# Kernel tuning notes

Measured on AMD Instinct MI355X. Metric: run time of the kernel, lower is better.

## Reference

```python
import jax, jax.numpy as jnp
import numpy as np

B, S, E, H = 2, 2048, 1024, 16
D = E // H  # head_dim = 64


def setup_inputs() -> dict:
    key = jax.random.key(0)
    ks = jax.random.split(key, 9)
    sc = 1.0 / np.sqrt(E)
    return {
        "x": jax.random.normal(ks[0], (B, S, E), dtype=jnp.float32),
        "Wq": jax.random.normal(ks[1], (E, E), dtype=jnp.float32) * sc,
        "bq": jnp.zeros((E,), dtype=jnp.float32),
        "Wk": jax.random.normal(ks[2], (E, E), dtype=jnp.float32) * sc,
        "bk": jnp.zeros((E,), dtype=jnp.float32),
        "Wv": jax.random.normal(ks[3], (E, E), dtype=jnp.float32) * sc,
        "bv": jnp.zeros((E,), dtype=jnp.float32),
        "Wo": jax.random.normal(ks[4], (E, E), dtype=jnp.float32) * sc,
        "bo": jnp.zeros((E,), dtype=jnp.float32),
    }


def reference(x, Wq, bq, Wk, bk, Wv, bv, Wo, bo):
    b, s, e = x.shape
    # projections: [B,S,E] -> [B,H,S,D]
    def heads(w, bias):
        return (x @ w + bias).reshape(b, s, H, D).transpose(0, 2, 1, 3)
    q, k, v = heads(Wq, bq), heads(Wk, bk), heads(Wv, bv)
    # scores [B,H,S,S]
    scores = jnp.einsum("bhqd,bhkd->bhqk", q, k) / jnp.sqrt(jnp.float32(D))
    causal = jnp.tril(jnp.ones((s, s), dtype=bool))
    scores = jnp.where(causal[None, None], scores, -jnp.inf)
    weights = jax.nn.softmax(scores, axis=-1)
    out = jnp.einsum("bhqk,bhkd->bhqd", weights, v)
    out = out.transpose(0, 2, 1, 3).reshape(b, s, e)
    return out @ Wo + bo
```

## Files before the change

kernel.cpp:

```cpp
#include <hip/hip_runtime.h>
#include <hip/hip_bf16.h>

#define B_SZ 2
#define S_LEN 2048
#define E_DIM 1024
#define NH 16
#define DH 64
#define M_ROWS (B_SZ * S_LEN)
#define QB 128
#define KVB 64

typedef __attribute__((ext_vector_type(8))) short short8;
typedef __attribute__((ext_vector_type(4))) float floatx4;

static __device__ __forceinline__ unsigned short f2bf(float f) {
    __hip_bfloat16 h = __float2bfloat16(f);
    return *reinterpret_cast<unsigned short*>(&h);
}
static __device__ __forceinline__ float bf2f(unsigned short u) {
    unsigned int v = ((unsigned int)u) << 16;
    return __builtin_bit_cast(float, v);
}

static __device__ __forceinline__ void gl2lds16(const void* g, void* l) {
    __builtin_amdgcn_global_load_lds((const __attribute__((address_space(1))) void*)g,
                                     (__attribute__((address_space(3))) void*)l, 16, 0, 0);
}

__global__ __launch_bounds__(256) void cvt_f32_bf16(const float* __restrict__ x,
                                                    unsigned short* __restrict__ y, int n) {
    int i = (blockIdx.x * 256 + threadIdx.x) * 4;
    if (i >= n) return;
    float4 v = *reinterpret_cast<const float4*>(x + i);
    ushort4 o;
    o.x = f2bf(v.x); o.y = f2bf(v.y); o.z = f2bf(v.z); o.w = f2bf(v.w);
    *reinterpret_cast<ushort4*>(y + i) = o;
}

__global__ __launch_bounds__(256) void transpose_w4(const float* __restrict__ W0,
                                                    const float* __restrict__ W1,
                                                    const float* __restrict__ W2,
                                                    const float* __restrict__ W3,
                                                    unsigned short* __restrict__ T0,
                                                    unsigned short* __restrict__ T1,
                                                    unsigned short* __restrict__ T2,
                                                    unsigned short* __restrict__ T3) {
    __shared__ float tile[32][33];
    int z = blockIdx.z;
    const float* W = (z == 0) ? W0 : (z == 1) ? W1 : (z == 2) ? W2 : W3;
    unsigned short* Wt = (z == 0) ? T0 : (z == 1) ? T1 : (z == 2) ? T2 : T3;
    int tx = threadIdx.x, ty = threadIdx.y;
    int bx = blockIdx.x * 32, by = blockIdx.y * 32;
#pragma unroll
    for (int i = 0; i < 32; i += 8)
        tile[ty + i][tx] = W[(size_t)(by + ty + i) * E_DIM + bx + tx];
    __syncthreads();
#pragma unroll
    for (int i = 0; i < 32; i += 8)
        Wt[(size_t)(bx + ty + i) * E_DIM + by + tx] = f2bf(tile[tx][ty + i]);
}

template <int NI>
static __device__ __forceinline__ void gemm_tile_mainloop(
    const unsigned short* __restrict__ A, const unsigned short* __restrict__ Bt,
    int mBase, int nBase, char* ldsA, char* ldsB, floatx4 (&acc)[4][NI]) {
    const int K = E_DIM;
    int t = threadIdx.x;
    int w = t >> 6, lane = t & 63;
    int lr = lane & 15, lh = lane >> 4;
    int wm = w >> 1, wn = w & 1;
    const char* Ab = (const char*)A;
    const char* Bb = (const char*)Bt;
    int srow = t >> 3;
    int scb = ((t & 7) << 4) ^ ((srow & 7) << 4);

#pragma unroll
    for (int mi = 0; mi < 4; mi++)
#pragma unroll
        for (int ni = 0; ni < NI; ni++) acc[mi][ni] = (floatx4){0.f, 0.f, 0.f, 0.f};

    for (int kt = 0; kt < K / 64; ++kt) {
        int k0 = kt * 64;
#pragma unroll
        for (int i = 0; i < 4; i++)
            gl2lds16(Ab + (size_t)(mBase + i * 32 + srow) * (K * 2) + k0 * 2 + scb,
                     ldsA + i * 4096 + t * 16);
#pragma unroll
        for (int i = 0; i < NI; i++)
            gl2lds16(Bb + (size_t)(nBase + i * 32 + srow) * (K * 2) + k0 * 2 + scb,
                     ldsB + i * 4096 + t * 16);
        __syncthreads();
#pragma unroll
        for (int ks = 0; ks < 2; ks++) {
            short8 af[4], bf[NI];
#pragma unroll
            for (int mi = 0; mi < 4; mi++) {
                int row = wm * 64 + mi * 16 + lr;
                af[mi] = *reinterpret_cast<const short8*>(
                    ldsA + ((row * 128 + ks * 64 + lh * 16) ^ ((row & 7) << 4)));
            }
#pragma unroll
            for (int ni = 0; ni < NI; ni++) {
                int row = wn * (NI * 16) + ni * 16 + lr;
                bf[ni] = *reinterpret_cast<const short8*>(
                    ldsB + ((row * 128 + ks * 64 + lh * 16) ^ ((row & 7) << 4)));
            }
#pragma unroll
            for (int mi = 0; mi < 4; mi++)
#pragma unroll
                for (int ni = 0; ni < NI; ni++)
                    acc[mi][ni] = __builtin_amdgcn_mfma_f32_16x16x32_bf16(af[mi], bf[ni],
                                                                          acc[mi][ni], 0, 0, 0);
        }
        __syncthreads();
    }
}

#define QSCALE 0.18033688011112042f

__global__ __launch_bounds__(256) void gemm_qkv(const unsigned short* __restrict__ Xb,
                                                const unsigned short* __restrict__ Wqt,
                                                const unsigned short* __restrict__ Wkt,
                                                const unsigned short* __restrict__ Wvt,
                                                const float* __restrict__ bq,
                                                const float* __restrict__ bk,
                                                const float* __restrict__ bv,
                                                unsigned short* __restrict__ Qg,
                                                unsigned short* __restrict__ Kg,
                                                unsigned short* __restrict__ Vtg) {
    __shared__ __align__(16) char smem[34816];
    char* ldsA = smem;
    char* ldsB = smem + 16384;

    int bid = blockIdx.y * 24 + blockIdx.x;
    int xcd = bid & 7, ii = bid >> 3;
    int lx = ii % 12, ly = ii / 12;
    int xx = (xcd & 1) * 12 + lx;
    int yy = ((xcd >> 1) << 3) + ly;
    int wsel = xx >> 3;
    int nBase = (xx & 7) << 7;
    int mBase = yy << 7;
    const unsigned short* Bt = (wsel == 0) ? Wqt : (wsel == 1) ? Wkt : Wvt;
    const float* bias = (wsel == 0) ? bq : (wsel == 1) ? bk : bv;

    floatx4 acc[4][4];
    gemm_tile_mainloop<4>(Xb, Bt, mBase, nBase, ldsA, ldsB, acc);

    int w = threadIdx.x >> 6, lane = threadIdx.x & 63;
    int lr = lane & 15, lh = lane >> 4;
    int wm = w >> 1, wn = w & 1;
    int b_ = mBase >> 11, s0 = mBase & (S_LEN - 1);

    if (wsel == 2) {
#pragma unroll
        for (int mi = 0; mi < 4; mi++) {
            int s_ = s0 + wm * 64 + mi * 16 + lh * 4;
#pragma unroll
            for (int ni = 0; ni < 4; ni++) {
                int nl = nBase + wn * 64 + ni * 16 + lr;
                int h = nl >> 6, d = nl & 63;
                float bb = bias[nl];
                ushort4 pk;
                pk.x = f2bf(acc[mi][ni][0] + bb);
                pk.y = f2bf(acc[mi][ni][1] + bb);
                pk.z = f2bf(acc[mi][ni][2] + bb);
                pk.w = f2bf(acc[mi][ni][3] + bb);
                *reinterpret_cast<ushort4*>(
                    &Vtg[((size_t)(b_ * NH + h) * DH + d) * S_LEN + s_]) = pk;
            }
        }
    } else {
        unsigned short* et = reinterpret_cast<unsigned short*>(smem);
        unsigned short* O = wsel ? Kg : Qg;
        float scale = wsel ? 1.0f : QSCALE;
#pragma unroll
        for (int mi = 0; mi < 4; mi++)
#pragma unroll
            for (int ni = 0; ni < 4; ni++) {
                int nl = wn * 64 + ni * 16 + lr;
                float bb = bias[nBase + nl];
#pragma unroll
                for (int r = 0; r < 4; r++) {
                    int ml = wm * 64 + mi * 16 + lh * 4 + r;
                    int q = ((ml >> 2) & 3) << 3;
                    et[ml * 136 + (nl ^ q)] = f2bf((acc[mi][ni][r] + bb) * scale);
                }
            }
        __syncthreads();
#pragma unroll
        for (int c = 0; c < 8; c++) {
            int id = c * 256 + threadIdx.x;
            int ml = id >> 4, nc = id & 15;
            int q = ((ml >> 2) & 3) << 3;
            short8 vv = *reinterpret_cast<const short8*>(&et[ml * 136 + ((nc * 8) ^ q)]);
            int n = nBase + nc * 8;
            int h = n >> 6, d = n & 63;
            *reinterpret_cast<short8*>(
                &O[((size_t)(b_ * NH + h) * S_LEN + (s0 + ml)) * DH + d]) = vv;
        }
    }
}

__global__ __launch_bounds__(256) void gemm_o(const unsigned short* __restrict__ Og,
                                              const unsigned short* __restrict__ Wot,
                                              const float* __restrict__ bo,
                                              float* __restrict__ out) {
    __shared__ __align__(16) char ldsA[16384];
    __shared__ __align__(16) char ldsB[8192];
    int bid = blockIdx.y * 16 + blockIdx.x;
    int xcd = bid & 7, ii = bid >> 3;
    int xx = ii & 15;
    int yy = (xcd << 2) | (ii >> 4);
    int nBase = xx << 6;
    int mBase = yy << 7;

    floatx4 acc[4][2];
    gemm_tile_mainloop<2>(Og, Wot, mBase, nBase, ldsA, ldsB, acc);

    int w = threadIdx.x >> 6, lane = threadIdx.x & 63;
    int lr = lane & 15, lh = lane >> 4;
    int wm = w >> 1, wn = w & 1;
#pragma unroll
    for (int mi = 0; mi < 4; mi++)
#pragma unroll
        for (int ni = 0; ni < 2; ni++)
#pragma unroll
            for (int r = 0; r < 4; r++) {
                int m = mBase + wm * 64 + mi * 16 + lh * 4 + r;
                int n = nBase + wn * 32 + ni * 16 + lr;
                out[(size_t)m * E_DIM + n] = acc[mi][ni][r] + bo[n];
            }
}

__global__ __launch_bounds__(256) void attn_fwd(const unsigned short* __restrict__ Qg,
                                                const unsigned short* __restrict__ Kg,
                                                const unsigned short* __restrict__ Vtg,
                                                unsigned short* __restrict__ Og,
                                                unsigned short* __restrict__ Opart,
                                                float* __restrict__ lpart) {
    __shared__ __align__(16) char kt_lds[2][KVB * 128];
    __shared__ __align__(16) char vt_lds[2][KVB * 128];
    __shared__ __align__(16) unsigned short p_lds[4][32][72];

    int bid = blockIdx.y * 24 + blockIdx.x;
    int xcd = bid & 7, ii = bid >> 3;
    int idx = ii % 24;
    int bh = (xcd << 2) + ii / 24;

    int qb, kt_lo, kt_hi, chunk;
    bool split;
    if (idx < 16) {
        split = true;
        qb = 8 + (idx & 7);
        chunk = idx >> 3;
        if (chunk == 0) { kt_lo = 0; kt_hi = qb; }
        else            { kt_lo = qb + 1; kt_hi = 2 * qb + 1; }
    } else {
        split = false; chunk = 0;
        qb = 23 - idx;
        kt_lo = 0; kt_hi = 2 * qb + 1;
    }

    int w = threadIdx.x >> 6, lane = threadIdx.x & 63;
    int lr = lane & 15, lh = lane >> 4;
    int q0 = qb * QB + w * 32;

    const char* Kb = (const char*)(Kg + (size_t)bh * S_LEN * DH);
    const char* Vb = (const char*)(Vtg + (size_t)bh * DH * S_LEN);
    const unsigned short* Qb = Qg + (size_t)bh * S_LEN * DH;

    int wi0 = w * 2;
    int srow0 = wi0 * 8 + (lane >> 3);
    int scol = (lane & 7) << 4;

    auto stage = [&](int buf, int kt) {
        int kv0 = kt * KVB;
#pragma unroll
        for (int i = 0; i < 2; ++i) {
            int row = srow0 + i * 8;
            int colb = scol ^ ((row & 7) << 4);
            gl2lds16(Kb + (size_t)(kv0 + row) * 128 + colb,
                     kt_lds[buf] + (wi0 + i) * 1024);
            gl2lds16(Vb + (size_t)row * (S_LEN * 2) + (size_t)kv0 * 2 + colb,
                     vt_lds[buf] + (wi0 + i) * 1024);
        }
    };

    short8 aq[2][2];
#pragma unroll
    for (int m = 0; m < 2; m++)
#pragma unroll
        for (int ks = 0; ks < 2; ks++)
            aq[m][ks] = *reinterpret_cast<const short8*>(
                Qb + (size_t)(q0 + m * 16 + lr) * DH + ks * 32 + lh * 8);

    floatx4 oacc[2][4];
    float lsum[2][4];
#pragma unroll
    for (int m = 0; m < 2; m++) {
#pragma unroll
        for (int dt = 0; dt < 4; dt++) oacc[m][dt] = (floatx4){0.f, 0.f, 0.f, 0.f};
#pragma unroll
        for (int r = 0; r < 4; r++) lsum[m][r] = 0.f;
    }

    stage(0, kt_lo);
    __syncthreads();
    int buf = 0;

    for (int kt = kt_lo; kt <= kt_hi; ++kt) {
        if (kt < kt_hi) stage(buf ^ 1, kt + 1);
        int kv0 = kt * KVB;
        bool skip = (kv0 > q0 + 31);
        if (!skip) {
            const char* Kt = kt_lds[buf];
            const char* Vt = vt_lds[buf];
            floatx4 sacc[2][4];
#pragma unroll
            for (int m = 0; m < 2; m++)
#pragma unroll
                for (int nt = 0; nt < 4; nt++) sacc[m][nt] = (floatx4){0.f, 0.f, 0.f, 0.f};
#pragma unroll
            for (int ks = 0; ks < 2; ks++)
#pragma unroll
                for (int nt = 0; nt < 4; nt++) {
                    int row = nt * 16 + lr;
                    int addr = (row * 128 + ks * 64 + lh * 16) ^ ((row & 7) << 4);
                    short8 bk = *reinterpret_cast<const short8*>(Kt + addr);
#pragma unroll
                    for (int m = 0; m < 2; m++)
                        sacc[m][nt] = __builtin_amdgcn_mfma_f32_16x16x32_bf16(
                            aq[m][ks], bk, sacc[m][nt], 0, 0, 0);
                }
            if (kv0 + KVB - 1 > q0) {
#pragma unroll
                for (int m = 0; m < 2; m++)
#pragma unroll
                    for (int nt = 0; nt < 4; nt++)
#pragma unroll
                        for (int r = 0; r < 4; r++) {
                            int qrow = q0 + m * 16 + lh * 4 + r;
                            int kcol = kv0 + nt * 16 + lr;
                            if (kcol > qrow) sacc[m][nt][r] = -1e30f;
                        }
            }
#pragma unroll
            for (int m = 0; m < 2; m++) {
                float rs[4] = {0.f, 0.f, 0.f, 0.f};
#pragma unroll
                for (int nt = 0; nt < 4; nt++)
#pragma unroll
                    for (int r = 0; r < 4; r++) {
                        float p = __builtin_amdgcn_exp2f(sacc[m][nt][r]);
                        rs[r] += p;
                        p_lds[w][m * 16 + lh * 4 + r][nt * 16 + lr] = f2bf(p);
                    }
#pragma unroll
                for (int r = 0; r < 4; r++) lsum[m][r] += rs[r];
            }
            asm volatile("s_waitcnt lgkmcnt(0)" ::: "memory");
            short8 pa[2][2];
#pragma unroll
            for (int m = 0; m < 2; m++)
#pragma unroll
                for (int ks = 0; ks < 2; ks++)
                    pa[m][ks] = *reinterpret_cast<const short8*>(
                        &p_lds[w][m * 16 + lr][ks * 32 + lh * 8]);
#pragma unroll
            for (int ks = 0; ks < 2; ks++)
#pragma unroll
                for (int dt = 0; dt < 4; dt++) {
                    int row = dt * 16 + lr;
                    int addr = (row * 128 + ks * 64 + lh * 16) ^ ((row & 7) << 4);
                    short8 bv = *reinterpret_cast<const short8*>(Vt + addr);
#pragma unroll
                    for (int m = 0; m < 2; m++)
                        oacc[m][dt] = __builtin_amdgcn_mfma_f32_16x16x32_bf16(
                            pa[m][ks], bv, oacc[m][dt], 0, 0, 0);
                }
        }
        __syncthreads();
        buf ^= 1;
    }

#pragma unroll
    for (int m = 0; m < 2; m++)
#pragma unroll
        for (int msk = 1; msk < 16; msk <<= 1)
#pragma unroll
            for (int r = 0; r < 4; r++) lsum[m][r] += __shfl_xor(lsum[m][r], msk);

    if (split) {
        int pi = ((bh << 3) + (qb - 8)) * 2 + chunk;
        unsigned short* Op = Opart + (size_t)pi * (QB * DH);
        float* lp = lpart + (size_t)pi * QB;
#pragma unroll
        for (int m = 0; m < 2; m++) {
#pragma unroll
            for (int r = 0; r < 4; r++) {
                int row = w * 32 + m * 16 + lh * 4 + r;
#pragma unroll
                for (int dt = 0; dt < 4; dt++)
                    Op[row * DH + dt * 16 + lr] = f2bf(oacc[m][dt][r]);
                if (lr == r) lp[row] = lsum[m][r];
            }
        }
    } else {
        int b_ = bh >> 4, h_ = bh & 15;
#pragma unroll
        for (int m = 0; m < 2; m++)
#pragma unroll
            for (int r = 0; r < 4; r++) {
                float inv = 1.f / lsum[m][r];
                int srow = q0 + m * 16 + lh * 4 + r;
#pragma unroll
                for (int dt = 0; dt < 4; dt++)
                    Og[((size_t)b_ * S_LEN + srow) * E_DIM + h_ * 64 + dt * 16 + lr] =
                        f2bf(oacc[m][dt][r] * inv);
            }
    }
}

__global__ __launch_bounds__(256) void attn_reduce(const unsigned short* __restrict__ Opart,
                                                   const float* __restrict__ lpart,
                                                   unsigned short* __restrict__ Og) {
    int bh = blockIdx.x;
    int qt = blockIdx.y;
    int t = threadIdx.x;
    int cg = t & 7, r0 = t >> 3;
    int pi0 = ((bh << 3) + qt) * 2;
    const unsigned short* A = Opart + (size_t)pi0 * (QB * DH);
    const unsigned short* Bp = A + (QB * DH);
    const float* lA = lpart + (size_t)pi0 * QB;
    const float* lB = lA + QB;
    int b_ = bh >> 4, h_ = bh & 15;
    int qrow0 = (8 + qt) * QB;
#pragma unroll
    for (int rr = 0; rr < 4; rr++) {
        int row = r0 + rr * 32;
        float inv = 1.f / (lA[row] + lB[row]);
        short8 va = *reinterpret_cast<const short8*>(A + row * DH + cg * 8);
        short8 vb = *reinterpret_cast<const short8*>(Bp + row * DH + cg * 8);
        short8 o;
#pragma unroll
        for (int j = 0; j < 8; j++)
            o[j] = (short)f2bf((bf2f((unsigned short)va[j]) + bf2f((unsigned short)vb[j])) * inv);
        *reinterpret_cast<short8*>(Og + ((size_t)b_ * S_LEN + qrow0 + row) * E_DIM +
                                   h_ * 64 + cg * 8) = o;
    }
}

extern "C" void kernel_launch(void* const* d_in, const int* in_sizes, int n_in,
                              void* d_out, int out_size, void* d_ws, size_t ws_size,
                              hipStream_t stream) {
    const float* x  = (const float*)d_in[0];
    const float* Wq = (const float*)d_in[1];
    const float* bq = (const float*)d_in[2];
    const float* Wk = (const float*)d_in[3];
    const float* bk = (const float*)d_in[4];
    const float* Wv = (const float*)d_in[5];
    const float* bv = (const float*)d_in[6];
    const float* Wo = (const float*)d_in[7];
    const float* bo = (const float*)d_in[8];
    float* out = (float*)d_out;

    const size_t NX = (size_t)M_ROWS * E_DIM;
    const size_t NW = (size_t)E_DIM * E_DIM;
    unsigned short* ws  = (unsigned short*)d_ws;
    unsigned short* Xb  = ws;
    unsigned short* Wqt = Xb + NX;
    unsigned short* Wkt = Wqt + NW;
    unsigned short* Wvt = Wkt + NW;
    unsigned short* Wot = Wvt + NW;
    unsigned short* Qg  = Wot + NW;
    unsigned short* Kg  = Qg + NX;
    unsigned short* Vtg = Kg + NX;
    unsigned short* Og  = Vtg + NX;
    unsigned short* Opart = Og + NX;
    float* lpart = (float*)(Opart + (size_t)512 * QB * DH);

    cvt_f32_bf16<<<dim3((unsigned)(NX / (256 * 4))), dim3(256), 0, stream>>>(x, Xb, (int)NX);
    transpose_w4<<<dim3(32, 32, 4), dim3(32, 8), 0, stream>>>(Wq, Wk, Wv, Wo,
                                                              Wqt, Wkt, Wvt, Wot);

    gemm_qkv<<<dim3(24, M_ROWS / 128), 256, 0, stream>>>(Xb, Wqt, Wkt, Wvt, bq, bk, bv,
                                                         Qg, Kg, Vtg);

    attn_fwd<<<dim3(24, B_SZ * NH), 256, 0, stream>>>(Qg, Kg, Vtg, Og, Opart, lpart);
    attn_reduce<<<dim3(B_SZ * NH, 8), 256, 0, stream>>>(Opart, lpart, Og);

    gemm_o<<<dim3(E_DIM / 64, M_ROWS / 128), 256, 0, stream>>>(Og, Wot, bo, out);
}
```

Baseline: 116.1 us.

## Fuse prep kernels and rewrite QKV GEMM with 256x256 double-buffered tiles

Merges the x conversion and the weight transpose into one prep launch. Replaces the QKV projection with a 512-thread kernel that computes Wcat·X^T in 256x256 tiles, using double-buffered LDS with the next tile's global loads interleaved between MFMA phases. It relies on Wqt/Wkt/Wvt being contiguous in the workspace so they act as one concatenated weight matrix. The larger tiles raise data reuse and cut the launch count, at the cost of 128KB of LDS, more registers, only 192 blocks, and new epilogue paths for the Q/K and transposed V layouts.

```diff
diff --git a/kernel.cpp b/kernel.cpp
--- a/kernel.cpp
+++ b/kernel.cpp
@@ -27,30 +27,36 @@
                                      (__attribute__((address_space(3))) void*)l, 16, 0, 0);
 }
 
-__global__ __launch_bounds__(256) void cvt_f32_bf16(const float* __restrict__ x,
-                                                    unsigned short* __restrict__ y, int n) {
-    int i = (blockIdx.x * 256 + threadIdx.x) * 4;
-    if (i >= n) return;
-    float4 v = *reinterpret_cast<const float4*>(x + i);
-    ushort4 o;
-    o.x = f2bf(v.x); o.y = f2bf(v.y); o.z = f2bf(v.z); o.w = f2bf(v.w);
-    *reinterpret_cast<ushort4*>(y + i) = o;
-}
-
-__global__ __launch_bounds__(256) void transpose_w4(const float* __restrict__ W0,
-                                                    const float* __restrict__ W1,
-                                                    const float* __restrict__ W2,
-                                                    const float* __restrict__ W3,
-                                                    unsigned short* __restrict__ T0,
-                                                    unsigned short* __restrict__ T1,
-                                                    unsigned short* __restrict__ T2,
-                                                    unsigned short* __restrict__ T3) {
+#define WAIT_VM0() asm volatile("s_waitcnt vmcnt(0)" ::: "memory")
+#define WAIT_LGKM0() asm volatile("s_waitcnt lgkmcnt(0)" ::: "memory")
+
+__global__ __launch_bounds__(256) void prep(const float* __restrict__ x,
+                                            unsigned short* __restrict__ Xb,
+                                            const float* __restrict__ W0,
+                                            const float* __restrict__ W1,
+                                            const float* __restrict__ W2,
+                                            const float* __restrict__ W3,
+                                            unsigned short* __restrict__ T0,
+                                            unsigned short* __restrict__ T1,
+                                            unsigned short* __restrict__ T2,
+                                            unsigned short* __restrict__ T3) {
     __shared__ float tile[32][33];
-    int z = blockIdx.z;
+    int bid = blockIdx.x;
+    int t = threadIdx.x;
+    if (bid < 4096) {
+        int i = (bid * 256 + t) * 4;
+        float4 v = *reinterpret_cast<const float4*>(x + i);
+        ushort4 o;
+        o.x = f2bf(v.x); o.y = f2bf(v.y); o.z = f2bf(v.z); o.w = f2bf(v.w);
+        *reinterpret_cast<ushort4*>(Xb + i) = o;
+        return;
+    }
+    int u = bid - 4096;
+    int z = u >> 10, rest = u & 1023;
+    int bx = (rest & 31) * 32, by = (rest >> 5) * 32;
     const float* W = (z == 0) ? W0 : (z == 1) ? W1 : (z == 2) ? W2 : W3;
     unsigned short* Wt = (z == 0) ? T0 : (z == 1) ? T1 : (z == 2) ? T2 : T3;
-    int tx = threadIdx.x, ty = threadIdx.y;
-    int bx = blockIdx.x * 32, by = blockIdx.y * 32;
+    int tx = t & 31, ty = t >> 5;
 #pragma unroll
     for (int i = 0; i < 32; i += 8)
         tile[ty + i][tx] = W[(size_t)(by + ty + i) * E_DIM + bx + tx];
@@ -58,6 +64,189 @@
 #pragma unroll
     for (int i = 0; i < 32; i += 8)
         Wt[(size_t)(bx + ty + i) * E_DIM + by + tx] = f2bf(tile[tx][ty + i]);
+}
+
+#define QSCALE 0.18033688011112042f
+
+__global__ __launch_bounds__(512, 2) void gemm_qkv8(const unsigned short* __restrict__ Wcat,
+                                                    const unsigned short* __restrict__ Xb,
+                                                    const float* __restrict__ bq,
+                                                    const float* __restrict__ bk,
+                                                    const float* __restrict__ bv,
+                                                    unsigned short* __restrict__ Qg,
+                                                    unsigned short* __restrict__ Kg,
+                                                    unsigned short* __restrict__ Vtg) {
+    __shared__ __align__(16) char lds[2][2][32768];
+
+    int t = threadIdx.x;
+    int b = blockIdx.x;
+    int xcd = b & 7, ii = b >> 3;
+    int it = (xcd & 3) * 3 + (ii >> 3);
+    int jt = (xcd >> 2) * 8 + (ii & 7);
+    int iBase = it << 8, jBase = jt << 8;
+
+    int w = t >> 6, lane = t & 63;
+    int lr = lane & 15, lh = lane >> 4;
+    int wm = w >> 2, wn = w & 3;
+
+    int srow = t >> 3;
+    int scbx = ((t & 7) << 4) ^ ((srow & 7) << 4);
+
+    const char* Ab = (const char*)Wcat;
+    const char* Bb = (const char*)Xb;
+
+    floatx4 acc[8][4];
+#pragma unroll
+    for (int i = 0; i < 8; i++)
+#pragma unroll
+        for (int j = 0; j < 4; j++) acc[i][j] = (floatx4){0.f, 0.f, 0.f, 0.f};
+
+    auto stageA = [&](int buf, int kt) {
+        int k0b = kt << 7;
+#pragma unroll
+        for (int c = 0; c < 4; c++)
+            gl2lds16(Ab + (size_t)(iBase + c * 64 + srow) * 2048 + k0b + scbx,
+                     &lds[buf][0][c * 8192 + t * 16]);
+    };
+    auto stageB = [&](int buf, int kt) {
+        int k0b = kt << 7;
+#pragma unroll
+        for (int c = 0; c < 4; c++)
+            gl2lds16(Bb + (size_t)(jBase + c * 64 + srow) * 2048 + k0b + scbx,
+                     &lds[buf][1][c * 8192 + t * 16]);
+    };
+
+    short8 af[4][2], bf[4][2];
+    auto rdA = [&](int buf, int qm) {
+#pragma unroll
+        for (int mi = 0; mi < 4; mi++)
+#pragma unroll
+            for (int ks = 0; ks < 2; ks++) {
+                int row = wm * 128 + qm * 64 + mi * 16 + lr;
+                af[mi][ks] = *reinterpret_cast<const short8*>(
+                    &lds[buf][0][(row * 128 + ks * 64 + lh * 16) ^ ((row & 7) << 4)]);
+            }
+    };
+    auto rdB = [&](int buf, int qn) {
+#pragma unroll
+        for (int ni = 0; ni < 2; ni++)
+#pragma unroll
+            for (int ks = 0; ks < 2; ks++) {
+                int row = wn * 64 + qn * 32 + ni * 16 + lr;
+                bf[qn * 2 + ni][ks] = *reinterpret_cast<const short8*>(
+                    &lds[buf][1][(row * 128 + ks * 64 + lh * 16) ^ ((row & 7) << 4)]);
+            }
+    };
+    auto mfma16 = [&](int qm, int qn) {
+        __builtin_amdgcn_s_setprio(1);
+#pragma unroll
+        for (int mi = 0; mi < 4; mi++)
+#pragma unroll
+            for (int ni = 0; ni < 2; ni++)
+#pragma unroll
+                for (int ks = 0; ks < 2; ks++)
+                    acc[qm * 4 + mi][qn * 2 + ni] = __builtin_amdgcn_mfma_f32_16x16x32_bf16(
+                        af[mi][ks], bf[qn * 2 + ni][ks], acc[qm * 4 + mi][qn * 2 + ni], 0, 0, 0);
+        __builtin_amdgcn_s_setprio(0);
+    };
+
+    const int NT = 16;
+    stageA(0, 0);
+    stageB(0, 0);
+    WAIT_VM0();
+    __builtin_amdgcn_s_barrier();
+
+    for (int kt = 0; kt < NT; ++kt) {
+        int cur = kt & 1, nxt = cur ^ 1;
+        bool pf = (kt + 1 < NT);
+        rdA(cur, 0);
+        rdB(cur, 0);
+        if (pf) stageA(nxt, kt + 1);
+        __builtin_amdgcn_s_barrier();
+        WAIT_LGKM0();
+        __builtin_amdgcn_sched_barrier(0);
+        mfma16(0, 0);
+        __builtin_amdgcn_s_barrier();
+        rdB(cur, 1);
+        if (pf) stageB(nxt, kt + 1);
+        __builtin_amdgcn_s_barrier();
+        WAIT_LGKM0();
+        __builtin_amdgcn_sched_barrier(0);
+        mfma16(0, 1);
+        __builtin_amdgcn_s_barrier();
+        rdA(cur, 1);
+        __builtin_amdgcn_s_barrier();
+        WAIT_LGKM0();
+        __builtin_amdgcn_sched_barrier(0);
+        mfma16(1, 0);
+        __builtin_amdgcn_s_barrier();
+        if (pf) WAIT_VM0();
+        __builtin_amdgcn_s_barrier();
+        mfma16(1, 1);
+        __builtin_amdgcn_s_barrier();
+    }
+
+    int wsel = iBase >> 10;
+    const float* bias = (wsel == 0) ? bq : (wsel == 1) ? bk : bv;
+    __syncthreads();
+
+    if (wsel < 2) {
+        unsigned short* O = wsel ? Kg : Qg;
+        float scale = wsel ? 1.0f : QSCALE;
+#pragma unroll
+        for (int mi8 = 0; mi8 < 8; mi8++) {
+            int i = iBase + wm * 128 + mi8 * 16 + lh * 4;
+            int im = i & 1023;
+            int h = im >> 6, d0 = im & 63;
+            float4 bs = *reinterpret_cast<const float4*>(&bias[im]);
+#pragma unroll
+            for (int nf = 0; nf < 4; nf++) {
+                int j = jBase + wn * 64 + nf * 16 + lr;
+                int b_ = j >> 11, s = j & (S_LEN - 1);
+                ushort4 pk;
+                pk.x = f2bf((acc[mi8][nf][0] + bs.x) * scale);
+                pk.y = f2bf((acc[mi8][nf][1] + bs.y) * scale);
+                pk.z = f2bf((acc[mi8][nf][2] + bs.z) * scale);
+                pk.w = f2bf((acc[mi8][nf][3] + bs.w) * scale);
+                *reinterpret_cast<ushort4*>(
+                    &O[((size_t)(b_ * NH + h) * S_LEN + s) * DH + d0]) = pk;
+            }
+        }
+    } else {
+        char* lw = &lds[0][0][0] + w * 16384;
+#pragma unroll
+        for (int mi8 = 0; mi8 < 8; mi8++) {
+            int i = iBase + wm * 128 + mi8 * 16 + lh * 4;
+            float4 bs = *reinterpret_cast<const float4*>(&bias[i & 1023]);
+#pragma unroll
+            for (int nf = 0; nf < 4; nf++) {
+                int jl = nf * 16 + lr;
+#pragma unroll
+                for (int r = 0; r < 4; r++) {
+                    int il = mi8 * 16 + lh * 4 + r;
+                    float bb = (r == 0) ? bs.x : (r == 1) ? bs.y : (r == 2) ? bs.z : bs.w;
+                    *reinterpret_cast<unsigned short*>(
+                        lw + ((il * 128 + jl * 2) ^ ((il & 7) << 4))) =
+                        f2bf(acc[mi8][nf][r] + bb);
+                }
+            }
+        }
+        __syncthreads();
+#pragma unroll
+        for (int rep = 0; rep < 16; rep++) {
+            int idx = rep * 64 + lane;
+            int il = idx >> 3, jb = idx & 7;
+            short8 vv = *reinterpret_cast<const short8*>(
+                lw + ((il * 128 + jb * 16) ^ ((il & 7) << 4)));
+            int i = iBase + wm * 128 + il;
+            int im = i & 1023;
+            int h = im >> 6, d = im & 63;
+            int j = jBase + wn * 64 + jb * 8;
+            int b_ = j >> 11, s = j & (S_LEN - 1);
+            *reinterpret_cast<short8*>(
+                &Vtg[((size_t)(b_ * NH + h) * DH + d) * S_LEN + s]) = vv;
+        }
+    }
 }
 
 template <int NI>
@@ -92,7 +281,7 @@
         __syncthreads();
 #pragma unroll
         for (int ks = 0; ks < 2; ks++) {
-            short8 af[4], bf[NI];
+            short8 af[4], bfr[NI];
 #pragma unroll
             for (int mi = 0; mi < 4; mi++) {
                 int row = wm * 64 + mi * 16 + lr;
@@ -102,102 +291,17 @@
 #pragma unroll
             for (int ni = 0; ni < NI; ni++) {
                 int row = wn * (NI * 16) + ni * 16 + lr;
-                bf[ni] = *reinterpret_cast<const short8*>(
+                bfr[ni] = *reinterpret_cast<const short8*>(
                     ldsB + ((row * 128 + ks * 64 + lh * 16) ^ ((row & 7) << 4)));
             }
 #pragma unroll
             for (int mi = 0; mi < 4; mi++)
 #pragma unroll
                 for (int ni = 0; ni < NI; ni++)
-                    acc[mi][ni] = __builtin_amdgcn_mfma_f32_16x16x32_bf16(af[mi], bf[ni],
+                    acc[mi][ni] = __builtin_amdgcn_mfma_f32_16x16x32_bf16(af[mi], bfr[ni],
                                                                           acc[mi][ni], 0, 0, 0);
         }
         __syncthreads();
-    }
-}
-
-#define QSCALE 0.18033688011112042f
-
-__global__ __launch_bounds__(256) void gemm_qkv(const unsigned short* __restrict__ Xb,
-                                                const unsigned short* __restrict__ Wqt,
-                                                const unsigned short* __restrict__ Wkt,
-                                                const unsigned short* __restrict__ Wvt,
-                                                const float* __restrict__ bq,
-                                                const float* __restrict__ bk,
-                                                const float* __restrict__ bv,
-                                                unsigned short* __restrict__ Qg,
-                                                unsigned short* __restrict__ Kg,
-                                                unsigned short* __restrict__ Vtg) {
-    __shared__ __align__(16) char smem[34816];
-    char* ldsA = smem;
-    char* ldsB = smem + 16384;
-
-    int bid = blockIdx.y * 24 + blockIdx.x;
-    int xcd = bid & 7, ii = bid >> 3;
-    int lx = ii % 12, ly = ii / 12;
-    int xx = (xcd & 1) * 12 + lx;
-    int yy = ((xcd >> 1) << 3) + ly;
-    int wsel = xx >> 3;
-    int nBase = (xx & 7) << 7;
-    int mBase = yy << 7;
-    const unsigned short* Bt = (wsel == 0) ? Wqt : (wsel == 1) ? Wkt : Wvt;
-    const float* bias = (wsel == 0) ? bq : (wsel == 1) ? bk : bv;
-
-    floatx4 acc[4][4];
-    gemm_tile_mainloop<4>(Xb, Bt, mBase, nBase, ldsA, ldsB, acc);
-
-    int w = threadIdx.x >> 6, lane = threadIdx.x & 63;
-    int lr = lane & 15, lh = lane >> 4;
-    int wm = w >> 1, wn = w & 1;
-    int b_ = mBase >> 11, s0 = mBase & (S_LEN - 1);
-
-    if (wsel == 2) {
-#pragma unroll
-        for (int mi = 0; mi < 4; mi++) {
-            int s_ = s0 + wm * 64 + mi * 16 + lh * 4;
-#pragma unroll
-            for (int ni = 0; ni < 4; ni++) {
-                int nl = nBase + wn * 64 + ni * 16 + lr;
-                int h = nl >> 6, d = nl & 63;
-                float bb = bias[nl];
-                ushort4 pk;
-                pk.x = f2bf(acc[mi][ni][0] + bb);
-                pk.y = f2bf(acc[mi][ni][1] + bb);
-                pk.z = f2bf(acc[mi][ni][2] + bb);
-                pk.w = f2bf(acc[mi][ni][3] + bb);
-                *reinterpret_cast<ushort4*>(
-                    &Vtg[((size_t)(b_ * NH + h) * DH + d) * S_LEN + s_]) = pk;
-            }
-        }
-    } else {
-        unsigned short* et = reinterpret_cast<unsigned short*>(smem);
-        unsigned short* O = wsel ? Kg : Qg;
-        float scale = wsel ? 1.0f : QSCALE;
-#pragma unroll
-        for (int mi = 0; mi < 4; mi++)
-#pragma unroll
-            for (int ni = 0; ni < 4; ni++) {
-                int nl = wn * 64 + ni * 16 + lr;
-                float bb = bias[nBase + nl];
-#pragma unroll
-                for (int r = 0; r < 4; r++) {
-                    int ml = wm * 64 + mi * 16 + lh * 4 + r;
-                    int q = ((ml >> 2) & 3) << 3;
-                    et[ml * 136 + (nl ^ q)] = f2bf((acc[mi][ni][r] + bb) * scale);
-                }
-            }
-        __syncthreads();
-#pragma unroll
-        for (int c = 0; c < 8; c++) {
-            int id = c * 256 + threadIdx.x;
-            int ml = id >> 4, nc = id & 15;
-            int q = ((ml >> 2) & 3) << 3;
-            short8 vv = *reinterpret_cast<const short8*>(&et[ml * 136 + ((nc * 8) ^ q)]);
-            int n = nBase + nc * 8;
-            int h = n >> 6, d = n & 63;
-            *reinterpret_cast<short8*>(
-                &O[((size_t)(b_ * NH + h) * S_LEN + (s0 + ml)) * DH + d]) = vv;
-        }
     }
 }
 
@@ -358,7 +462,7 @@
 #pragma unroll
                 for (int r = 0; r < 4; r++) lsum[m][r] += rs[r];
             }
-            asm volatile("s_waitcnt lgkmcnt(0)" ::: "memory");
+            WAIT_LGKM0();
             short8 pa[2][2];
 #pragma unroll
             for (int m = 0; m < 2; m++)
@@ -479,12 +583,9 @@
     unsigned short* Opart = Og + NX;
     float* lpart = (float*)(Opart + (size_t)512 * QB * DH);
 
-    cvt_f32_bf16<<<dim3((unsigned)(NX / (256 * 4))), dim3(256), 0, stream>>>(x, Xb, (int)NX);
-    transpose_w4<<<dim3(32, 32, 4), dim3(32, 8), 0, stream>>>(Wq, Wk, Wv, Wo,
-                                                              Wqt, Wkt, Wvt, Wot);
-
-    gemm_qkv<<<dim3(24, M_ROWS / 128), 256, 0, stream>>>(Xb, Wqt, Wkt, Wvt, bq, bk, bv,
-                                                         Qg, Kg, Vtg);
+    prep<<<dim3(8192), 256, 0, stream>>>(x, Xb, Wq, Wk, Wv, Wo, Wqt, Wkt, Wvt, Wot);
+
+    gemm_qkv8<<<dim3(192), 512, 0, stream>>>(Wqt, Xb, bq, bk, bv, Qg, Kg, Vtg);
 
     attn_fwd<<<dim3(24, B_SZ * NH), 256, 0, stream>>>(Qg, Kg, Vtg, Og, Opart, lpart);
     attn_reduce<<<dim3(B_SZ * NH, 8), 256, 0, stream>>>(Opart, lpart, Og);
```

After: 109.1 us. 1.06x faster.
